# Kernel tuning notes

Hardware: AMD Instinct MI355X
Metric: run time of the kernel (lower is better)

The kernel has to match this reference:

```python
import jax, jax.numpy as jnp
import numpy as np

B, D_IN, D_OUT, M = 4096, 1024, 1024, 16
GAMMA = 2.0


def setup_inputs() -> dict:
    key = jax.random.key(0)
    ks = jax.random.split(key, 5)
    scale_in = 1.0 / np.sqrt(D_IN)
    return {
        "x": jax.random.normal(ks[0], (B, D_IN), dtype=jnp.float32),
        "W": jax.random.normal(ks[1], (M, D_IN, D_OUT), dtype=jnp.float32) * scale_in,
        "b": jax.random.normal(ks[2], (M, D_OUT), dtype=jnp.float32) * 0.01,
        "Wg": jax.random.normal(ks[3], (D_IN, M), dtype=jnp.float32) * scale_in,
        "bg": jax.random.normal(ks[4], (M,), dtype=jnp.float32) * 0.01,
    }


def reference(x, W, b, Wg, bg):
    # Gate: linear -> pow(gamma) -> normalize by row sum -> relu
    gu = x @ Wg + bg                                   # [B, M]
    gp = jnp.power(gu, GAMMA)                          # gamma = 2.0
    gates = jax.nn.relu(gp / jnp.sum(gp, axis=1, keepdims=True))  # [B, M]
    # M dense expert modules: relu(x @ W_m + b_m), gated and summed (AdditionSublayer)
    h = jax.nn.relu(jnp.einsum("bi,mio->bmo", x, W) + b)          # [B, M, D_OUT]
    return jnp.einsum("bm,bmo->bo", gates, h)                     # [B, D_OUT]
```

## Files before the change

kernel.cpp:

```cpp
#include <hip/hip_runtime.h>

typedef unsigned short u16;
typedef __attribute__((ext_vector_type(4))) float f32x4;
typedef __attribute__((ext_vector_type(8))) short bf16x8;
typedef __attribute__((ext_vector_type(4))) unsigned short u16x4;

#define NT 128

__device__ __forceinline__ u16 f2bf(float f) {
  union { float f; unsigned u; } v; v.f = f;
  unsigned r = v.u + 0x7FFFu + ((v.u >> 16) & 1u);
  return (u16)(r >> 16);
}

__device__ __forceinline__ f32x4 zero4() {
  f32x4 z; z.x = 0.f; z.y = 0.f; z.z = 0.f; z.w = 0.f; return z;
}

__global__ __launch_bounds__(256) void k_cvt_x2(const float* __restrict__ x, u16* __restrict__ xb2) {
  int g = blockIdx.x * 256 + threadIdx.x;
  int lane = g & 63;
  int kk = (g >> 6) & 1;
  int kt = (g >> 7) & 15;
  int gb = g >> 11;
  int row = gb * 16 + (lane & 15);
  int k0 = kt * 64 + kk * 32 + (lane >> 4) * 8;
  const f32x4* src = (const f32x4*)(x + (size_t)row * 1024 + k0);
  f32x4 v0 = src[0], v1 = src[1];
  union { u16 u[8]; bf16x8 v; } o;
  o.u[0]=f2bf(v0.x); o.u[1]=f2bf(v0.y); o.u[2]=f2bf(v0.z); o.u[3]=f2bf(v0.w);
  o.u[4]=f2bf(v1.x); o.u[5]=f2bf(v1.y); o.u[6]=f2bf(v1.z); o.u[7]=f2bf(v1.w);
  ((bf16x8*)xb2)[g] = o.v;
}

__global__ __launch_bounds__(256) void k_tw(const float* __restrict__ W, u16* __restrict__ wt) {
  __shared__ float t[64][65];
  int bid = blockIdx.x;
  int e = bid >> 8, rem = bid & 255, kt = rem >> 4, nt = rem & 15;
  int tid = threadIdx.x;
  int c = tid & 63, r0 = tid >> 6;
  const float* src = W + (size_t)e * 1048576 + (size_t)(kt * 64) * 1024 + nt * 64;
  #pragma unroll
  for (int p = 0; p < 16; ++p) {
    int r = r0 + p * 4;
    t[r][c] = src[r * 1024 + c];
  }
  __syncthreads();
  u16* dst = wt + (size_t)e * 1048576 + (size_t)(nt * 64) * 1024 + kt * 64;
  #pragma unroll
  for (int p = 0; p < 16; ++p) {
    int r2 = r0 + p * 4;
    dst[r2 * 1024 + c] = f2bf(t[c][r2]);
  }
}

__global__ __launch_bounds__(256) void k_gates(const float* __restrict__ x, const float* __restrict__ Wg,
                                               const float* __restrict__ bg, float* __restrict__ gates) {
  int wid = threadIdx.x >> 6, lane = threadIdx.x & 63;
  int b = blockIdx.x * 4 + wid;
  const float* xr = x + (size_t)b * 1024;
  float acc[16];
  #pragma unroll
  for (int m = 0; m < 16; ++m) acc[m] = 0.f;
  for (int i = lane; i < 1024; i += 64) {
    float xv = xr[i];
    const f32x4* wg = (const f32x4*)(Wg + (size_t)i * 16);
    #pragma unroll
    for (int q = 0; q < 4; ++q) {
      f32x4 w = wg[q];
      acc[q*4+0] += xv * w.x; acc[q*4+1] += xv * w.y;
      acc[q*4+2] += xv * w.z; acc[q*4+3] += xv * w.w;
    }
  }
  #pragma unroll
  for (int m = 0; m < 16; ++m) {
    #pragma unroll
    for (int off = 32; off > 0; off >>= 1)
      acc[m] += __shfl_xor(acc[m], off, 64);
  }
  float tot = 0.f, gp[16];
  #pragma unroll
  for (int m = 0; m < 16; ++m) { float gu = acc[m] + bg[m]; gp[m] = gu * gu; tot += gp[m]; }
  float inv = 1.f / tot;
  if (lane == 0) {
    #pragma unroll
    for (int m = 0; m < 16; ++m) gates[(size_t)b * 16 + m] = gp[m] * inv;
  }
}

#define GLL(srcaddr, ldsaddr) \
  __builtin_amdgcn_global_load_lds((const __attribute__((address_space(1))) void*)(srcaddr), \
                                   (__attribute__((address_space(3))) void*)(ldsaddr), 16, 0, 0)

#define MFMA16(A0,A1,A2,A3,B0,B1,B2,B3) do { \
  acc[0][0] = __builtin_amdgcn_mfma_f32_16x16x32_bf16(A0, B0, acc[0][0], 0,0,0); \
  acc[0][1] = __builtin_amdgcn_mfma_f32_16x16x32_bf16(A0, B1, acc[0][1], 0,0,0); \
  acc[0][2] = __builtin_amdgcn_mfma_f32_16x16x32_bf16(A0, B2, acc[0][2], 0,0,0); \
  acc[0][3] = __builtin_amdgcn_mfma_f32_16x16x32_bf16(A0, B3, acc[0][3], 0,0,0); \
  acc[1][0] = __builtin_amdgcn_mfma_f32_16x16x32_bf16(A1, B0, acc[1][0], 0,0,0); \
  acc[1][1] = __builtin_amdgcn_mfma_f32_16x16x32_bf16(A1, B1, acc[1][1], 0,0,0); \
  acc[1][2] = __builtin_amdgcn_mfma_f32_16x16x32_bf16(A1, B2, acc[1][2], 0,0,0); \
  acc[1][3] = __builtin_amdgcn_mfma_f32_16x16x32_bf16(A1, B3, acc[1][3], 0,0,0); \
  acc[2][0] = __builtin_amdgcn_mfma_f32_16x16x32_bf16(A2, B0, acc[2][0], 0,0,0); \
  acc[2][1] = __builtin_amdgcn_mfma_f32_16x16x32_bf16(A2, B1, acc[2][1], 0,0,0); \
  acc[2][2] = __builtin_amdgcn_mfma_f32_16x16x32_bf16(A2, B2, acc[2][2], 0,0,0); \
  acc[2][3] = __builtin_amdgcn_mfma_f32_16x16x32_bf16(A2, B3, acc[2][3], 0,0,0); \
  acc[3][0] = __builtin_amdgcn_mfma_f32_16x16x32_bf16(A3, B0, acc[3][0], 0,0,0); \
  acc[3][1] = __builtin_amdgcn_mfma_f32_16x16x32_bf16(A3, B1, acc[3][1], 0,0,0); \
  acc[3][2] = __builtin_amdgcn_mfma_f32_16x16x32_bf16(A3, B2, acc[3][2], 0,0,0); \
  acc[3][3] = __builtin_amdgcn_mfma_f32_16x16x32_bf16(A3, B3, acc[3][3], 0,0,0); \
} while (0)

__global__ __launch_bounds__(256, 2)
void k_moe(const u16* __restrict__ xb2, const u16* __restrict__ wt,
           const float* __restrict__ gates, const float* __restrict__ bias,
           float* __restrict__ out0, float* __restrict__ p1out) {
  __shared__ __align__(16) u16 sB[2 * 8192];
  __shared__ float lgat[1024];
  __shared__ float lbias[1024];

  int tid = threadIdx.x;
  int bid = blockIdx.x;
  int swz = (bid & 7) * 64 + (bid >> 3);
  int btile = swz & 31;
  int pnl = swz >> 5;
  int ntile = pnl & 7;
  int grp = pnl >> 3;
  int brow0 = btile * 128;
  int ncol0 = ntile * 128;
  int mb = grp * 8;

  int wid = tid >> 6, lane = tid & 63;
  int wm = wid >> 1, wn = wid & 1;
  int lrow = lane & 15, lk = lane >> 4;
  int sw = lrow & 7;

  const u16* bsrc = wt + (size_t)mb * 1048576 + (size_t)ncol0 * 1024;

  int sg[4], ldd[4];
  #pragma unroll
  for (int it = 0; it < 4; ++it) {
    int idx = it * 256 + tid;
    int r = idx >> 3, s = idx & 7;
    sg[it] = r * 1024 + (s ^ (r & 7)) * 8;
    ldd[it] = (it * 256 + wid * 64) * 8;
  }

  int baseB = (wn * 64 + lrow) * 64;
  int pb0 = baseB + ((0 + lk) ^ sw) * 8;
  int pb1 = baseB + ((4 + lk) ^ sw) * 8;

  const u16* ab0 = xb2 + (size_t)(btile * 8 + wm * 4 + 0) * 16384 + lane * 8;
  const u16* ab1 = ab0 + 16384;
  const u16* ab2 = ab0 + 32768;
  const u16* ab3 = ab0 + 49152;

  f32x4 acc[4][4], oacc[4][4];
  #pragma unroll
  for (int i = 0; i < 4; ++i)
    #pragma unroll
    for (int j = 0; j < 4; ++j) { acc[i][j] = zero4(); oacc[i][j] = zero4(); }

  u16 *b0 = sB, *b1 = sB + 8192;

  bf16x8 fa0, fa1, fa2, fa3, ga0, ga1, ga2, ga3;
  fa0 = *(const bf16x8*)(ab0);       ga0 = *(const bf16x8*)(ab0 + 512);
  fa1 = *(const bf16x8*)(ab1);       ga1 = *(const bf16x8*)(ab1 + 512);
  fa2 = *(const bf16x8*)(ab2);       ga2 = *(const bf16x8*)(ab2 + 512);
  fa3 = *(const bf16x8*)(ab3);       ga3 = *(const bf16x8*)(ab3 + 512);
  #pragma unroll
  for (int it = 0; it < 4; ++it) GLL(bsrc + sg[it], b0 + ldd[it]);
  #pragma unroll
  for (int i = 0; i < 4; ++i) {
    int idx = i * 256 + tid;
    lgat[idx] = gates[(size_t)(brow0 + (idx & 127)) * 16 + mb + (idx >> 7)];
  }
  #pragma unroll
  for (int i = 0; i < 4; ++i) {
    int idx = i * 256 + tid;
    lbias[idx] = bias[(size_t)(mb + (idx >> 7)) * 1024 + ncol0 + (idx & 127)];
  }
  asm volatile("s_waitcnt vmcnt(0)" ::: "memory");
  __builtin_amdgcn_s_barrier();
  __builtin_amdgcn_sched_barrier(0);

  for (int t = 0; t < NT; ++t) {
    bool pf = (t + 1 < NT);
    bf16x8 b00, b01, b02, b03, b10, b11, b12, b13;

    b00 = *(const bf16x8*)&b0[pb0];
    b01 = *(const bf16x8*)&b0[pb0 + 1024];
    b02 = *(const bf16x8*)&b0[pb0 + 2048];
    b03 = *(const bf16x8*)&b0[pb0 + 3072];
    b10 = *(const bf16x8*)&b0[pb1];
    b11 = *(const bf16x8*)&b0[pb1 + 1024];
    b12 = *(const bf16x8*)&b0[pb1 + 2048];
    b13 = *(const bf16x8*)&b0[pb1 + 3072];

    if (pf) {
      const u16* sb1 = bsrc + (size_t)((t + 1) >> 4) * 1048576 + ((t + 1) & 15) * 64;
      #pragma unroll
      for (int it = 0; it < 4; ++it) GLL(sb1 + sg[it], b1 + ldd[it]);
    }

    __builtin_amdgcn_s_setprio(1);
    MFMA16(fa0, fa1, fa2, fa3, b00, b01, b02, b03);
    MFMA16(ga0, ga1, ga2, ga3, b10, b11, b12, b13);
    __builtin_amdgcn_s_setprio(0);
    __builtin_amdgcn_sched_barrier(0);

    if (pf) {
      int ko = ((t + 1) & 15) * 1024;
      fa0 = *(const bf16x8*)(ab0 + ko);       ga0 = *(const bf16x8*)(ab0 + ko + 512);
      fa1 = *(const bf16x8*)(ab1 + ko);       ga1 = *(const bf16x8*)(ab1 + ko + 512);
      fa2 = *(const bf16x8*)(ab2 + ko);       ga2 = *(const bf16x8*)(ab2 + ko + 512);
      fa3 = *(const bf16x8*)(ab3 + ko);       ga3 = *(const bf16x8*)(ab3 + ko + 512);
    }

    if ((t & 15) == 15) {
      int ml = t >> 4;
      float bvv[4];
      #pragma unroll
      for (int ni = 0; ni < 4; ++ni) bvv[ni] = lbias[ml * 128 + wn * 64 + ni * 16 + lrow];
      #pragma unroll
      for (int mi = 0; mi < 4; ++mi) {
        f32x4 gv = *(const f32x4*)&lgat[ml * 128 + wm * 64 + mi * 16 + lk * 4];
        #pragma unroll
        for (int ni = 0; ni < 4; ++ni) {
          #pragma unroll
          for (int j = 0; j < 4; ++j) {
            float h = acc[mi][ni][j] + bvv[ni];
            h = fmaxf(h, 0.f);
            oacc[mi][ni][j] += gv[j] * h;
          }
          acc[mi][ni] = zero4();
        }
      }
    }

    if (pf) {
      asm volatile("s_waitcnt vmcnt(8)" ::: "memory");
      __builtin_amdgcn_s_barrier();
      __builtin_amdgcn_sched_barrier(0);
      u16* tb = b0; b0 = b1; b1 = tb;
    }
  }

  float* op = grp ? p1out : out0;
  #pragma unroll
  for (int mi = 0; mi < 4; ++mi)
    #pragma unroll
    for (int j = 0; j < 4; ++j) {
      int row = brow0 + wm * 64 + mi * 16 + lk * 4 + j;
      #pragma unroll
      for (int ni = 0; ni < 4; ++ni) {
        int col = ncol0 + wn * 64 + ni * 16 + lrow;
        op[(size_t)row * 1024 + col] = oacc[mi][ni][j];
      }
    }
}

__global__ __launch_bounds__(256) void k_add(float* __restrict__ out, const float* __restrict__ p1) {
  int i = blockIdx.x * 256 + threadIdx.x;
  f32x4 a = ((const f32x4*)out)[i];
  f32x4 b = ((const f32x4*)p1)[i];
  ((f32x4*)out)[i] = a + b;
}

extern "C" void kernel_launch(void* const* d_in, const int* in_sizes, int n_in,
                              void* d_out, int out_size, void* d_ws, size_t ws_size,
                              hipStream_t stream) {
  const float* x  = (const float*)d_in[0];
  const float* W  = (const float*)d_in[1];
  const float* b  = (const float*)d_in[2];
  const float* Wg = (const float*)d_in[3];
  const float* bg = (const float*)d_in[4];
  float* out = (float*)d_out;

  char* ws = (char*)d_ws;
  u16* xb2    = (u16*)ws;
  u16* wt     = (u16*)(ws + 8388608);
  float* gts  = (float*)(ws + 41943040);
  float* p1   = (float*)(ws + 42205184);

  k_cvt_x2<<<2048, 256, 0, stream>>>(x, xb2);
  k_tw<<<4096, 256, 0, stream>>>(W, wt);
  k_gates<<<1024, 256, 0, stream>>>(x, Wg, bg, gts);
  k_moe<<<512, 256, 0, stream>>>(xb2, wt, gts, b, out, p1);
  k_add<<<4096, 256, 0, stream>>>(out, p1);
}
```

Before: 206.7 us.

## Double-buffer A fragments in registers and unroll the main loop by two

Restructures the main K loop into a two-way unrolled macro with ping-pong A register fragments. The next A fragments are issued before the MFMAs instead of after them, and the second half of the B LDS reads is deferred until after the first 16 MFMAs. The prologue now stages gates and bias through registers and waits only on the A loads before the first barrier. The goal is better latency hiding of global A loads and LDS reads, at the cost of more VGPRs (an extra set of 8 bf16x8), which may pressure occupancy at launch_bounds(256,2).

```diff
diff --git a/kernel.cpp b/kernel.cpp
--- a/kernel.cpp
+++ b/kernel.cpp
@@ -92,23 +92,69 @@
   __builtin_amdgcn_global_load_lds((const __attribute__((address_space(1))) void*)(srcaddr), \
                                    (__attribute__((address_space(3))) void*)(ldsaddr), 16, 0, 0)
 
-#define MFMA16(A0,A1,A2,A3,B0,B1,B2,B3) do { \
-  acc[0][0] = __builtin_amdgcn_mfma_f32_16x16x32_bf16(A0, B0, acc[0][0], 0,0,0); \
-  acc[0][1] = __builtin_amdgcn_mfma_f32_16x16x32_bf16(A0, B1, acc[0][1], 0,0,0); \
-  acc[0][2] = __builtin_amdgcn_mfma_f32_16x16x32_bf16(A0, B2, acc[0][2], 0,0,0); \
-  acc[0][3] = __builtin_amdgcn_mfma_f32_16x16x32_bf16(A0, B3, acc[0][3], 0,0,0); \
-  acc[1][0] = __builtin_amdgcn_mfma_f32_16x16x32_bf16(A1, B0, acc[1][0], 0,0,0); \
-  acc[1][1] = __builtin_amdgcn_mfma_f32_16x16x32_bf16(A1, B1, acc[1][1], 0,0,0); \
-  acc[1][2] = __builtin_amdgcn_mfma_f32_16x16x32_bf16(A1, B2, acc[1][2], 0,0,0); \
-  acc[1][3] = __builtin_amdgcn_mfma_f32_16x16x32_bf16(A1, B3, acc[1][3], 0,0,0); \
-  acc[2][0] = __builtin_amdgcn_mfma_f32_16x16x32_bf16(A2, B0, acc[2][0], 0,0,0); \
-  acc[2][1] = __builtin_amdgcn_mfma_f32_16x16x32_bf16(A2, B1, acc[2][1], 0,0,0); \
-  acc[2][2] = __builtin_amdgcn_mfma_f32_16x16x32_bf16(A2, B2, acc[2][2], 0,0,0); \
-  acc[2][3] = __builtin_amdgcn_mfma_f32_16x16x32_bf16(A2, B3, acc[2][3], 0,0,0); \
-  acc[3][0] = __builtin_amdgcn_mfma_f32_16x16x32_bf16(A3, B0, acc[3][0], 0,0,0); \
-  acc[3][1] = __builtin_amdgcn_mfma_f32_16x16x32_bf16(A3, B1, acc[3][1], 0,0,0); \
-  acc[3][2] = __builtin_amdgcn_mfma_f32_16x16x32_bf16(A3, B2, acc[3][2], 0,0,0); \
-  acc[3][3] = __builtin_amdgcn_mfma_f32_16x16x32_bf16(A3, B3, acc[3][3], 0,0,0); \
+#define SUBITER(T, U, L, PF) do {                                              \
+  int _t = (T);                                                                \
+  bf16x8 cc[4];                                                                \
+  cc[0] = *(const bf16x8*)&b0[pb0];                                            \
+  cc[1] = *(const bf16x8*)&b0[pb0 + 1024];                                     \
+  cc[2] = *(const bf16x8*)&b0[pb0 + 2048];                                     \
+  cc[3] = *(const bf16x8*)&b0[pb0 + 3072];                                     \
+  if (PF) {                                                                    \
+    const u16* sb1 = bsrc + (size_t)((_t + 1) >> 4) * 1048576 + ((_t + 1) & 15) * 64; \
+    GLL(sb1 + sg[0], b1 + ldd[0]); GLL(sb1 + sg[1], b1 + ldd[1]);              \
+    GLL(sb1 + sg[2], b1 + ldd[2]); GLL(sb1 + sg[3], b1 + ldd[3]);              \
+  }                                                                            \
+  __builtin_amdgcn_sched_barrier(0);   \
+  if (PF) {                                                                    \
+    int ko = ((_t + 1) & 15) * 1024;                                           \
+    av[L][0] = *(const bf16x8*)(ab0 + ko); av[L][4] = *(const bf16x8*)(ab0 + ko + 512); \
+    av[L][1] = *(const bf16x8*)(ab1 + ko); av[L][5] = *(const bf16x8*)(ab1 + ko + 512); \
+    av[L][2] = *(const bf16x8*)(ab2 + ko); av[L][6] = *(const bf16x8*)(ab2 + ko + 512); \
+    av[L][3] = *(const bf16x8*)(ab3 + ko); av[L][7] = *(const bf16x8*)(ab3 + ko + 512); \
+  }                                                                            \
+  __builtin_amdgcn_s_setprio(1);                                               \
+  _Pragma("unroll")                                                            \
+  for (int mi = 0; mi < 4; ++mi)                                               \
+    _Pragma("unroll")                                                          \
+    for (int ni = 0; ni < 4; ++ni)                                             \
+      acc[mi][ni] = __builtin_amdgcn_mfma_f32_16x16x32_bf16(av[U][mi], cc[ni], acc[mi][ni], 0,0,0); \
+  cc[0] = *(const bf16x8*)&b0[pb1];                                            \
+  cc[1] = *(const bf16x8*)&b0[pb1 + 1024];                                     \
+  cc[2] = *(const bf16x8*)&b0[pb1 + 2048];                                     \
+  cc[3] = *(const bf16x8*)&b0[pb1 + 3072];                                     \
+  _Pragma("unroll")                                                            \
+  for (int mi = 0; mi < 4; ++mi)                                               \
+    _Pragma("unroll")                                                          \
+    for (int ni = 0; ni < 4; ++ni)                                             \
+      acc[mi][ni] = __builtin_amdgcn_mfma_f32_16x16x32_bf16(av[U][4 + mi], cc[ni], acc[mi][ni], 0,0,0); \
+  __builtin_amdgcn_s_setprio(0);                                               \
+  if ((_t & 15) == 15) {                                                       \
+    int ml = _t >> 4;                                                          \
+    float bvv[4];                                                              \
+    _Pragma("unroll")                                                          \
+    for (int ni = 0; ni < 4; ++ni) bvv[ni] = lbias[ml * 128 + wn * 64 + ni * 16 + lrow]; \
+    _Pragma("unroll")                                                          \
+    for (int mi = 0; mi < 4; ++mi) {                                           \
+      f32x4 gv = *(const f32x4*)&lgat[ml * 128 + wm * 64 + mi * 16 + lk * 4];  \
+      _Pragma("unroll")                                                        \
+      for (int ni = 0; ni < 4; ++ni) {                                         \
+        _Pragma("unroll")                                                      \
+        for (int j = 0; j < 4; ++j) {                                          \
+          float h = acc[mi][ni][j] + bvv[ni];                                  \
+          h = fmaxf(h, 0.f);                                                   \
+          oacc[mi][ni][j] += gv[j] * h;                                        \
+        }                                                                      \
+        acc[mi][ni] = zero4();                                                 \
+      }                                                                        \
+    }                                                                          \
+  }                                                                            \
+  if (PF) {                                                                    \
+       \
+    asm volatile("s_waitcnt vmcnt(8)" ::: "memory");                           \
+    __builtin_amdgcn_s_barrier();                                              \
+    __builtin_amdgcn_sched_barrier(0);                                         \
+    u16* _tb = b0; b0 = b1; b1 = _tb;                                          \
+  }                                                                            \
 } while (0)
 
 __global__ __launch_bounds__(256, 2)
@@ -162,89 +208,41 @@
     for (int j = 0; j < 4; ++j) { acc[i][j] = zero4(); oacc[i][j] = zero4(); }
 
   u16 *b0 = sB, *b1 = sB + 8192;
-
-  bf16x8 fa0, fa1, fa2, fa3, ga0, ga1, ga2, ga3;
-  fa0 = *(const bf16x8*)(ab0);       ga0 = *(const bf16x8*)(ab0 + 512);
-  fa1 = *(const bf16x8*)(ab1);       ga1 = *(const bf16x8*)(ab1 + 512);
-  fa2 = *(const bf16x8*)(ab2);       ga2 = *(const bf16x8*)(ab2 + 512);
-  fa3 = *(const bf16x8*)(ab3);       ga3 = *(const bf16x8*)(ab3 + 512);
-  #pragma unroll
-  for (int it = 0; it < 4; ++it) GLL(bsrc + sg[it], b0 + ldd[it]);
-  #pragma unroll
-  for (int i = 0; i < 4; ++i) {
-    int idx = i * 256 + tid;
-    lgat[idx] = gates[(size_t)(brow0 + (idx & 127)) * 16 + mb + (idx >> 7)];
-  }
-  #pragma unroll
-  for (int i = 0; i < 4; ++i) {
-    int idx = i * 256 + tid;
-    lbias[idx] = bias[(size_t)(mb + (idx >> 7)) * 1024 + ncol0 + (idx & 127)];
-  }
-  asm volatile("s_waitcnt vmcnt(0)" ::: "memory");
+  bf16x8 av[2][8];
+
+  {
+    float gt[4], bt[4];
+    #pragma unroll
+    for (int i = 0; i < 4; ++i) {
+      int idx = i * 256 + tid;
+      gt[i] = gates[(size_t)(brow0 + (idx & 127)) * 16 + mb + (idx >> 7)];
+      bt[i] = bias[(size_t)(mb + (idx >> 7)) * 1024 + ncol0 + (idx & 127)];
+    }
+    asm volatile("s_waitcnt vmcnt(0)" ::: "memory");
+    #pragma unroll
+    for (int i = 0; i < 4; ++i) {
+      int idx = i * 256 + tid;
+      lgat[idx] = gt[i];
+      lbias[idx] = bt[i];
+    }
+  }
+  GLL(bsrc + sg[0], b0 + ldd[0]); GLL(bsrc + sg[1], b0 + ldd[1]);
+  GLL(bsrc + sg[2], b0 + ldd[2]); GLL(bsrc + sg[3], b0 + ldd[3]);
+  __builtin_amdgcn_sched_barrier(0);
+  av[0][0] = *(const bf16x8*)(ab0); av[0][4] = *(const bf16x8*)(ab0 + 512);
+  av[0][1] = *(const bf16x8*)(ab1); av[0][5] = *(const bf16x8*)(ab1 + 512);
+  av[0][2] = *(const bf16x8*)(ab2); av[0][6] = *(const bf16x8*)(ab2 + 512);
+  av[0][3] = *(const bf16x8*)(ab3); av[0][7] = *(const bf16x8*)(ab3 + 512);
+  asm volatile("s_waitcnt vmcnt(8)" ::: "memory");
   __builtin_amdgcn_s_barrier();
   __builtin_amdgcn_sched_barrier(0);
 
-  for (int t = 0; t < NT; ++t) {
-    bool pf = (t + 1 < NT);
-    bf16x8 b00, b01, b02, b03, b10, b11, b12, b13;
-
-    b00 = *(const bf16x8*)&b0[pb0];
-    b01 = *(const bf16x8*)&b0[pb0 + 1024];
-    b02 = *(const bf16x8*)&b0[pb0 + 2048];
-    b03 = *(const bf16x8*)&b0[pb0 + 3072];
-    b10 = *(const bf16x8*)&b0[pb1];
-    b11 = *(const bf16x8*)&b0[pb1 + 1024];
-    b12 = *(const bf16x8*)&b0[pb1 + 2048];
-    b13 = *(const bf16x8*)&b0[pb1 + 3072];
-
-    if (pf) {
-      const u16* sb1 = bsrc + (size_t)((t + 1) >> 4) * 1048576 + ((t + 1) & 15) * 64;
-      #pragma unroll
-      for (int it = 0; it < 4; ++it) GLL(sb1 + sg[it], b1 + ldd[it]);
-    }
-
-    __builtin_amdgcn_s_setprio(1);
-    MFMA16(fa0, fa1, fa2, fa3, b00, b01, b02, b03);
-    MFMA16(ga0, ga1, ga2, ga3, b10, b11, b12, b13);
-    __builtin_amdgcn_s_setprio(0);
-    __builtin_amdgcn_sched_barrier(0);
-
-    if (pf) {
-      int ko = ((t + 1) & 15) * 1024;
-      fa0 = *(const bf16x8*)(ab0 + ko);       ga0 = *(const bf16x8*)(ab0 + ko + 512);
-      fa1 = *(const bf16x8*)(ab1 + ko);       ga1 = *(const bf16x8*)(ab1 + ko + 512);
-      fa2 = *(const bf16x8*)(ab2 + ko);       ga2 = *(const bf16x8*)(ab2 + ko + 512);
-      fa3 = *(const bf16x8*)(ab3 + ko);       ga3 = *(const bf16x8*)(ab3 + ko + 512);
-    }
-
-    if ((t & 15) == 15) {
-      int ml = t >> 4;
-      float bvv[4];
-      #pragma unroll
-      for (int ni = 0; ni < 4; ++ni) bvv[ni] = lbias[ml * 128 + wn * 64 + ni * 16 + lrow];
-      #pragma unroll
-      for (int mi = 0; mi < 4; ++mi) {
-        f32x4 gv = *(const f32x4*)&lgat[ml * 128 + wm * 64 + mi * 16 + lk * 4];
-        #pragma unroll
-        for (int ni = 0; ni < 4; ++ni) {
-          #pragma unroll
-          for (int j = 0; j < 4; ++j) {
-            float h = acc[mi][ni][j] + bvv[ni];
-            h = fmaxf(h, 0.f);
-            oacc[mi][ni][j] += gv[j] * h;
-          }
-          acc[mi][ni] = zero4();
-        }
-      }
-    }
-
-    if (pf) {
-      asm volatile("s_waitcnt vmcnt(8)" ::: "memory");
-      __builtin_amdgcn_s_barrier();
-      __builtin_amdgcn_sched_barrier(0);
-      u16* tb = b0; b0 = b1; b1 = tb;
-    }
-  }
+  for (int u = 0; u < NT / 2 - 1; ++u) {
+    SUBITER(2 * u,     0, 1, true);
+    SUBITER(2 * u + 1, 1, 0, true);
+  }
+  SUBITER(NT - 2, 0, 1, true);
+  SUBITER(NT - 1, 1, 0, false);
 
   float* op = grp ? p1out : out0;
   #pragma unroll
```

Measured after the change: 216.2 us. 4.6% more time.
